# Optimization experiments

Measured on AMD Instinct MI355X. Metric: run time of the kernel, lower is better.

The kernel has to match this reference:

```python
import jax, jax.numpy as jnp
import numpy as np

LORA_SCALING = 16.0 / 8.0  # lora_alpha / lora_r


def setup_inputs() -> dict:
    key = jax.random.key(0)
    k_x, k_m, k_wm, k_bm, k_wa, k_wb = jax.random.split(key, 6)
    B, S, D_in, D_out, R = 4, 2048, 4096, 4096, 8
    x = jax.random.normal(k_x, (B, S, D_in), dtype=jnp.float32)
    im_mask = jax.random.randint(k_m, (B, S), 0, 2) > 0  # bool token mask
    # Linear weights stored torch-style: [out, in]
    W_main = jax.random.normal(k_wm, (D_out, D_in), dtype=jnp.float32) * (1.0 / np.sqrt(D_in))
    b_main = jax.random.normal(k_bm, (D_out,), dtype=jnp.float32) * 0.01
    W_A = jax.random.normal(k_wa, (R, D_in), dtype=jnp.float32) * (1.0 / np.sqrt(D_in))
    W_B = jax.random.normal(k_wb, (D_out, R), dtype=jnp.float32) * (1.0 / np.sqrt(R))
    return {"x": x, "im_mask": im_mask, "W_main": W_main, "b_main": b_main, "W_A": W_A, "W_B": W_B}


def reference(x, im_mask, W_main, b_main, W_A, W_B):
    # Main dense path: res = x @ W_main.T + b
    res = jnp.einsum('bsd,od->bso', x, W_main) + b_main
    # LoRA path applied only at masked tokens (dropout disabled / eval):
    # res[im_mask] += (x[im_mask] @ W_A.T) @ W_B.T * scaling
    # Static-shape equivalent: compute everywhere, mask the add.
    lora = jnp.einsum('bsr,or->bso', jnp.einsum('bsd,rd->bsr', x, W_A), W_B)
    return res + jnp.where(im_mask[..., None], lora * LORA_SCALING, jnp.zeros((), x.dtype))
```

## Files before the change

kernel.cpp:

```cpp
#include <hip/hip_runtime.h>

typedef unsigned short u16;
typedef unsigned int   u32;
typedef unsigned long long u64;
typedef __bf16 bf16x8 __attribute__((ext_vector_type(8)));
typedef float  f32x4  __attribute__((ext_vector_type(4)));

#define AS1 __attribute__((address_space(1)))
#define AS3 __attribute__((address_space(3)))

#define M_TOK 8192
#define K_DIM 4096
#define N_DIM 4096
#define BK    32
#define NKT   (K_DIM / BK)

static __device__ __forceinline__ u16 f2bf(float f) {
  u32 u = __builtin_bit_cast(u32, f);
  return (u16)((u + (0x7FFFu + ((u >> 16) & 1u))) >> 16);
}

static __device__ __forceinline__ void gld_lds16(const void* g, void* l) {
  __builtin_amdgcn_global_load_lds((AS1 u32*)(u64)g, (AS3 u32*)(u32)(u64)l, 16, 0, 0);
}

__global__ __launch_bounds__(256) void k_prep(const float* __restrict__ x,
                                              const float* __restrict__ WA,
                                              const float* __restrict__ W,
                                              u16* __restrict__ xb,
                                              float* __restrict__ mid,
                                              u16* __restrict__ Wb) {
  const int t = threadIdx.x;
  if (blockIdx.x >= M_TOK) {
    const int cb = blockIdx.x - M_TOK;
    const float4* W4 = (const float4*)W;
    ushort4* Wb4 = (ushort4*)Wb;
    const int n4 = (N_DIM * K_DIM) / 4;
    int i = cb * 256 + t;
    for (; i < n4; i += 2048 * 256) {
      float4 v = W4[i];
      ushort4 o;
      o.x = f2bf(v.x); o.y = f2bf(v.y); o.z = f2bf(v.z); o.w = f2bf(v.w);
      Wb4[i] = o;
    }
    return;
  }
  const int m = blockIdx.x;
  const float4* xr = (const float4*)(x + (size_t)m * K_DIM);
  ushort4* xbr = (ushort4*)(xb + (size_t)m * K_DIM);
  float a[8] = {0.f,0.f,0.f,0.f,0.f,0.f,0.f,0.f};
  #pragma unroll
  for (int i = 0; i < 4; ++i) {
    const int k4 = t + i * 256;
    float4 v = xr[k4];
    ushort4 o;
    o.x = f2bf(v.x); o.y = f2bf(v.y); o.z = f2bf(v.z); o.w = f2bf(v.w);
    xbr[k4] = o;
    #pragma unroll
    for (int r = 0; r < 8; ++r) {
      float4 wv = ((const float4*)(WA + (size_t)r * K_DIM))[k4];
      a[r] += v.x * wv.x + v.y * wv.y + v.z * wv.z + v.w * wv.w;
    }
  }
  #pragma unroll
  for (int r = 0; r < 8; ++r) {
    #pragma unroll
    for (int off = 32; off > 0; off >>= 1)
      a[r] += __shfl_down(a[r], off);
  }
  __shared__ float red[4][8];
  const int w = t >> 6, l = t & 63;
  if (l == 0) {
    #pragma unroll
    for (int r = 0; r < 8; ++r) red[w][r] = a[r];
  }
  __syncthreads();
  if (t < 8)
    mid[(size_t)m * 8 + t] = 2.0f * (red[0][t] + red[1][t] + red[2][t] + red[3][t]);
}

__global__ __launch_bounds__(512, 2) void k_gemm(
    const u16* __restrict__ A, const u16* __restrict__ B,
    const float* __restrict__ bias, const int* __restrict__ mask,
    const float* __restrict__ mid, const float* __restrict__ WBw,
    float* __restrict__ out) {
  __shared__ u16 smem[4][2][256][BK];

  const int t = threadIdx.x;
  const int wid = t >> 6, l = t & 63;
  const int wr = wid >> 2, wc = wid & 3;
  const int fr = l & 15, fq = l >> 4;

  const int bid = blockIdx.x;
  const int swz = (bid & 7) * 64 + (bid >> 3);
  const int bm = swz >> 4, bn = swz & 15;

  const char* Ag = (const char*)(A + (size_t)bm * 256 * K_DIM);
  const char* Bg = (const char*)(B + (size_t)bn * 256 * K_DIM);
  const size_t rowb = (size_t)K_DIM * 2;

  const int srow = t >> 2;
  const int schk = (((t & 3) ^ ((t >> 3) & 3)) * 16);
  const char* bA0 = Ag + (size_t)srow * rowb + schk;
  const char* bA1 = Ag + (size_t)(128 + srow) * rowb + schk;
  const char* bB0 = Bg + (size_t)srow * rowb + schk;
  const char* bB1 = Bg + (size_t)(128 + srow) * rowb + schk;
  char* lbase = (char*)&smem[0][0][0][0] + wid * 1024;

  f32x4 acc[8][4];
  #pragma unroll
  for (int m = 0; m < 8; ++m)
    #pragma unroll
    for (int n = 0; n < 4; ++n)
      acc[m][n] = (f32x4){0.f, 0.f, 0.f, 0.f};

  #pragma unroll
  for (int pk = 0; pk < 3; ++pk) {
    gld_lds16(bA0 + pk * 64, lbase + pk * 32768);
    gld_lds16(bA1 + pk * 64, lbase + pk * 32768 + 8192);
    gld_lds16(bB0 + pk * 64, lbase + pk * 32768 + 16384);
    gld_lds16(bB1 + pk * 64, lbase + pk * 32768 + 24576);
  }
  asm volatile("s_waitcnt vmcnt(4)" ::: "memory");
  __builtin_amdgcn_s_barrier();

  const int csw = (fq ^ ((fr >> 1) & 3)) * 8;

  const char* gA0 = bA0 + 192;
  const char* gA1 = bA1 + 192;
  const char* gB0 = bB0 + 192;
  const char* gB1 = bB1 + 192;

  bf16x8 af[8], bfP[4], bfQ[4];

  {
    const u16* Ap_ = &smem[0][0][wr * 128 + fr][csw];
    const u16* Bp_ = &smem[0][1][wc * 64 + fr][csw];
    #pragma unroll
    for (int m = 0; m < 8; ++m) af[m] = *(const bf16x8*)(Ap_ + m * 16 * BK);
    #pragma unroll
    for (int n = 0; n < 4; ++n) bfP[n] = *(const bf16x8*)(Bp_ + n * 16 * BK);
  }

  #define K_TILE(RBUF, SB, DOSTAGE, DOREAD, GOFF, WAIT, BFC, BFN) do {       \
    if (DOSTAGE) {                                                           \
      gld_lds16(gA0 + (GOFF), lbase + (SB) * 32768);                         \
      gld_lds16(gA1 + (GOFF), lbase + (SB) * 32768 + 8192);                  \
      gld_lds16(gB0 + (GOFF), lbase + (SB) * 32768 + 16384);                 \
      gld_lds16(gB1 + (GOFF), lbase + (SB) * 32768 + 24576);                 \
    }                                                                        \
    __builtin_amdgcn_s_setprio(1);                                           \
    _Pragma("unroll")                                                        \
    for (int m = 0; m < 4; ++m)                                              \
      _Pragma("unroll")                                                      \
      for (int n = 0; n < 4; ++n)                                            \
        acc[m][n] = __builtin_amdgcn_mfma_f32_16x16x32_bf16(                 \
            af[m], BFC[n], acc[m][n], 0, 0, 0);                              \
    __builtin_amdgcn_s_setprio(0);                                           \
    if (DOREAD) {                                                            \
      const u16* Ap_ = &smem[RBUF][0][wr * 128 + fr][csw];                   \
      const u16* Bp_ = &smem[RBUF][1][wc * 64 + fr][csw];                    \
      _Pragma("unroll")                                                      \
      for (int m = 0; m < 4; ++m)                                            \
        af[m] = *(const bf16x8*)(Ap_ + m * 16 * BK);                         \
      _Pragma("unroll")                                                      \
      for (int n = 0; n < 4; ++n)                                            \
        BFN[n] = *(const bf16x8*)(Bp_ + n * 16 * BK);                        \
    }                                                                        \
    __builtin_amdgcn_sched_barrier(0);                                       \
    __builtin_amdgcn_s_setprio(1);                                           \
    _Pragma("unroll")                                                        \
    for (int m = 4; m < 8; ++m)                                              \
      _Pragma("unroll")                                                      \
      for (int n = 0; n < 4; ++n)                                            \
        acc[m][n] = __builtin_amdgcn_mfma_f32_16x16x32_bf16(                 \
            af[m], BFC[n], acc[m][n], 0, 0, 0);                              \
    __builtin_amdgcn_s_setprio(0);                                           \
    if (DOREAD) {                                                            \
      const u16* Ap_ = &smem[RBUF][0][wr * 128 + fr][csw];                   \
      _Pragma("unroll")                                                      \
      for (int m = 4; m < 8; ++m)                                            \
        af[m] = *(const bf16x8*)(Ap_ + m * 16 * BK);                         \
    }                                                                        \
    __builtin_amdgcn_sched_barrier(0);                                       \
    WAIT;                                                                    \
    __builtin_amdgcn_s_barrier();                                            \
  } while (0)

  #define VM4 asm volatile("s_waitcnt vmcnt(4)" ::: "memory")
  #define VM0 asm volatile("s_waitcnt vmcnt(0)" ::: "memory")
  #define NOW ((void)0)

  for (int ktb = 0; ktb < NKT - 4; ktb += 4) {
    K_TILE(1, 3, true, true, 0,   VM4, bfP, bfQ);
    K_TILE(2, 0, true, true, 64,  VM4, bfQ, bfP);
    K_TILE(3, 1, true, true, 128, VM4, bfP, bfQ);
    K_TILE(0, 2, true, true, 192, VM4, bfQ, bfP);
    gA0 += 256; gA1 += 256; gB0 += 256; gB1 += 256;
  }
  K_TILE(1, 3, true,  true,  0, VM4, bfP, bfQ);
  K_TILE(2, 0, false, true,  0, VM0, bfQ, bfP);
  K_TILE(3, 0, false, true,  0, NOW, bfP, bfQ);
  K_TILE(0, 0, false, false, 0, NOW, bfQ, bfP);

  #undef K_TILE
  #undef VM4
  #undef VM0
  #undef NOW

  const int gn0 = bn * 256 + wc * 64;
  const size_t gm0 = (size_t)bm * 256 + wr * 128;
  float wbv[4][8]; float bv[4];
  #pragma unroll
  for (int n = 0; n < 4; ++n) {
    const int gn = gn0 + n * 16 + fr;
    bv[n] = bias[gn];
    const float4 w0 = ((const float4*)(WBw + (size_t)gn * 8))[0];
    const float4 w1 = ((const float4*)(WBw + (size_t)gn * 8))[1];
    wbv[n][0] = w0.x; wbv[n][1] = w0.y; wbv[n][2] = w0.z; wbv[n][3] = w0.w;
    wbv[n][4] = w1.x; wbv[n][5] = w1.y; wbv[n][6] = w1.z; wbv[n][7] = w1.w;
  }
  #pragma unroll
  for (int m = 0; m < 8; ++m) {
    #pragma unroll
    for (int j = 0; j < 4; ++j) {
      const size_t gm = gm0 + m * 16 + fq * 4 + j;
      const int msk = mask[gm];
      const float4 m0 = ((const float4*)(mid + gm * 8))[0];
      const float4 m1 = ((const float4*)(mid + gm * 8))[1];
      float* orow = out + gm * (size_t)N_DIM;
      #pragma unroll
      for (int n = 0; n < 4; ++n) {
        const float lora =
            m0.x * wbv[n][0] + m0.y * wbv[n][1] + m0.z * wbv[n][2] + m0.w * wbv[n][3] +
            m1.x * wbv[n][4] + m1.y * wbv[n][5] + m1.z * wbv[n][6] + m1.w * wbv[n][7];
        orow[gn0 + n * 16 + fr] = acc[m][n][j] + bv[n] + (msk ? lora : 0.0f);
      }
    }
  }
}

extern "C" void kernel_launch(void* const* d_in, const int* in_sizes, int n_in,
                              void* d_out, int out_size, void* d_ws, size_t ws_size,
                              hipStream_t stream) {
  (void)in_sizes; (void)n_in; (void)out_size; (void)ws_size;
  const float* x     = (const float*)d_in[0];
  const int*   mask  = (const int*)d_in[1];
  const float* Wm    = (const float*)d_in[2];
  const float* bmain = (const float*)d_in[3];
  const float* WA    = (const float*)d_in[4];
  const float* WB    = (const float*)d_in[5];
  float* out = (float*)d_out;

  u16* xb  = (u16*)d_ws;
  u16* wb  = xb + (size_t)M_TOK * K_DIM;
  float* mid = (float*)(wb + (size_t)N_DIM * K_DIM);

  k_prep<<<M_TOK + 2048, 256, 0, stream>>>(x, WA, Wm, xb, mid, wb);
  dim3 grid((M_TOK / 256) * (N_DIM / 256));
  k_gemm<<<grid, 512, 0, stream>>>(xb, wb, bmain, mask, mid, WB, out);
}
```

Baseline: 331.2 us.

## Load B fragments directly from global into registers, stage only A through LDS

Stops staging the B (weight) tile through shared memory. Each wave now loads its own B MFMA fragments straight from global memory into registers, two K-tiles ahead, while A keeps its 4-buffer LDS pipeline. This halves LDS footprint and LDS read traffic, which should ease LDS bandwidth pressure and the occupancy limit. In exchange B is no longer shared across the two wave rows, so global and L2 traffic for B doubles, and the vmcnt wait accounting changes, which risks stalls or ordering errors.

```diff
diff --git a/kernel.cpp b/kernel.cpp
--- a/kernel.cpp
+++ b/kernel.cpp
@@ -84,7 +84,7 @@
     const float* __restrict__ bias, const int* __restrict__ mask,
     const float* __restrict__ mid, const float* __restrict__ WBw,
     float* __restrict__ out) {
-  __shared__ u16 smem[4][2][256][BK];
+  __shared__ u16 smem[4][256][BK];
 
   const int t = threadIdx.x;
   const int wid = t >> 6, l = t & 63;
@@ -101,11 +101,11 @@
 
   const int srow = t >> 2;
   const int schk = (((t & 3) ^ ((t >> 3) & 3)) * 16);
-  const char* bA0 = Ag + (size_t)srow * rowb + schk;
-  const char* bA1 = Ag + (size_t)(128 + srow) * rowb + schk;
-  const char* bB0 = Bg + (size_t)srow * rowb + schk;
-  const char* bB1 = Bg + (size_t)(128 + srow) * rowb + schk;
-  char* lbase = (char*)&smem[0][0][0][0] + wid * 1024;
+  const char* gA0 = Ag + (size_t)srow * rowb + schk;
+  const char* gA1 = Ag + (size_t)(128 + srow) * rowb + schk;
+  char* lbase = (char*)&smem[0][0][0] + wid * 1024;
+
+  const char* qB = Bg + (size_t)(wc * 64 + fr) * rowb + fq * 16;
 
   f32x4 acc[8][4];
   #pragma unroll
@@ -114,41 +114,43 @@
     for (int n = 0; n < 4; ++n)
       acc[m][n] = (f32x4){0.f, 0.f, 0.f, 0.f};
 
+  bf16x8 af[8], bfA[4], bfB[4];
+
   #pragma unroll
   for (int pk = 0; pk < 3; ++pk) {
-    gld_lds16(bA0 + pk * 64, lbase + pk * 32768);
-    gld_lds16(bA1 + pk * 64, lbase + pk * 32768 + 8192);
-    gld_lds16(bB0 + pk * 64, lbase + pk * 32768 + 16384);
-    gld_lds16(bB1 + pk * 64, lbase + pk * 32768 + 24576);
-  }
+    gld_lds16(gA0 + pk * 64, lbase + pk * 16384);
+    gld_lds16(gA1 + pk * 64, lbase + pk * 16384 + 8192);
+  }
+  __builtin_amdgcn_sched_barrier(0);
+  #pragma unroll
+  for (int n = 0; n < 4; ++n)
+    bfA[n] = *(const bf16x8*)(qB + (size_t)n * 16 * rowb);
+  __builtin_amdgcn_sched_barrier(0);
+  #pragma unroll
+  for (int n = 0; n < 4; ++n)
+    bfB[n] = *(const bf16x8*)(qB + (size_t)n * 16 * rowb + 64);
+  __builtin_amdgcn_sched_barrier(0);
   asm volatile("s_waitcnt vmcnt(4)" ::: "memory");
   __builtin_amdgcn_s_barrier();
 
   const int csw = (fq ^ ((fr >> 1) & 3)) * 8;
 
-  const char* gA0 = bA0 + 192;
-  const char* gA1 = bA1 + 192;
-  const char* gB0 = bB0 + 192;
-  const char* gB1 = bB1 + 192;
-
-  bf16x8 af[8], bfP[4], bfQ[4];
-
   {
-    const u16* Ap_ = &smem[0][0][wr * 128 + fr][csw];
-    const u16* Bp_ = &smem[0][1][wc * 64 + fr][csw];
+    const u16* Ap_ = &smem[0][wr * 128 + fr][csw];
     #pragma unroll
     for (int m = 0; m < 8; ++m) af[m] = *(const bf16x8*)(Ap_ + m * 16 * BK);
-    #pragma unroll
-    for (int n = 0; n < 4; ++n) bfP[n] = *(const bf16x8*)(Bp_ + n * 16 * BK);
-  }
-
-  #define K_TILE(RBUF, SB, DOSTAGE, DOREAD, GOFF, WAIT, BFC, BFN) do {       \
+  }
+
+  const char* pA0 = gA0 + 192;
+  const char* pA1 = gA1 + 192;
+  const char* pB  = qB + 128;
+
+  #define K_TILE(RBUF, SB, DOSTAGE, DOREAD, DOB, GOFF, BOFF, WAIT, BFC) do { \
     if (DOSTAGE) {                                                           \
-      gld_lds16(gA0 + (GOFF), lbase + (SB) * 32768);                         \
-      gld_lds16(gA1 + (GOFF), lbase + (SB) * 32768 + 8192);                  \
-      gld_lds16(gB0 + (GOFF), lbase + (SB) * 32768 + 16384);                 \
-      gld_lds16(gB1 + (GOFF), lbase + (SB) * 32768 + 24576);                 \
-    }                                                                        \
+      gld_lds16(pA0 + (GOFF), lbase + (SB) * 16384);                         \
+      gld_lds16(pA1 + (GOFF), lbase + (SB) * 16384 + 8192);                  \
+    }                                                                        \
+    __builtin_amdgcn_sched_barrier(0);                                       \
     __builtin_amdgcn_s_setprio(1);                                           \
     _Pragma("unroll")                                                        \
     for (int m = 0; m < 4; ++m)                                              \
@@ -158,14 +160,10 @@
             af[m], BFC[n], acc[m][n], 0, 0, 0);                              \
     __builtin_amdgcn_s_setprio(0);                                           \
     if (DOREAD) {                                                            \
-      const u16* Ap_ = &smem[RBUF][0][wr * 128 + fr][csw];                   \
-      const u16* Bp_ = &smem[RBUF][1][wc * 64 + fr][csw];                    \
+      const u16* Ap_ = &smem[RBUF][wr * 128 + fr][csw];                      \
       _Pragma("unroll")                                                      \
       for (int m = 0; m < 4; ++m)                                            \
         af[m] = *(const bf16x8*)(Ap_ + m * 16 * BK);                         \
-      _Pragma("unroll")                                                      \
-      for (int n = 0; n < 4; ++n)                                            \
-        BFN[n] = *(const bf16x8*)(Bp_ + n * 16 * BK);                        \
     }                                                                        \
     __builtin_amdgcn_sched_barrier(0);                                       \
     __builtin_amdgcn_s_setprio(1);                                           \
@@ -177,33 +175,41 @@
             af[m], BFC[n], acc[m][n], 0, 0, 0);                              \
     __builtin_amdgcn_s_setprio(0);                                           \
     if (DOREAD) {                                                            \
-      const u16* Ap_ = &smem[RBUF][0][wr * 128 + fr][csw];                   \
+      const u16* Ap_ = &smem[RBUF][wr * 128 + fr][csw];                      \
       _Pragma("unroll")                                                      \
       for (int m = 4; m < 8; ++m)                                            \
         af[m] = *(const bf16x8*)(Ap_ + m * 16 * BK);                         \
+    }                                                                        \
+    __builtin_amdgcn_sched_barrier(0);                                       \
+    if (DOB) {                                                               \
+      _Pragma("unroll")                                                      \
+      for (int n = 0; n < 4; ++n)                                            \
+        BFC[n] = *(const bf16x8*)(pB + (size_t)n * 16 * rowb + (BOFF));      \
     }                                                                        \
     __builtin_amdgcn_sched_barrier(0);                                       \
     WAIT;                                                                    \
     __builtin_amdgcn_s_barrier();                                            \
   } while (0)
 
+  #define VM6 asm volatile("s_waitcnt vmcnt(6)" ::: "memory")
   #define VM4 asm volatile("s_waitcnt vmcnt(4)" ::: "memory")
   #define VM0 asm volatile("s_waitcnt vmcnt(0)" ::: "memory")
   #define NOW ((void)0)
 
   for (int ktb = 0; ktb < NKT - 4; ktb += 4) {
-    K_TILE(1, 3, true, true, 0,   VM4, bfP, bfQ);
-    K_TILE(2, 0, true, true, 64,  VM4, bfQ, bfP);
-    K_TILE(3, 1, true, true, 128, VM4, bfP, bfQ);
-    K_TILE(0, 2, true, true, 192, VM4, bfQ, bfP);
-    gA0 += 256; gA1 += 256; gB0 += 256; gB1 += 256;
-  }
-  K_TILE(1, 3, true,  true,  0, VM4, bfP, bfQ);
-  K_TILE(2, 0, false, true,  0, VM0, bfQ, bfP);
-  K_TILE(3, 0, false, true,  0, NOW, bfP, bfQ);
-  K_TILE(0, 0, false, false, 0, NOW, bfQ, bfP);
+    K_TILE(1, 3, true, true, true, 0,   0,   VM6, bfA);
+    K_TILE(2, 0, true, true, true, 64,  64,  VM6, bfB);
+    K_TILE(3, 1, true, true, true, 128, 128, VM6, bfA);
+    K_TILE(0, 2, true, true, true, 192, 192, VM6, bfB);
+    pA0 += 256; pA1 += 256; pB += 256;
+  }
+  K_TILE(1, 3, true,  true,  true,  0, 0,   VM6, bfA);
+  K_TILE(2, 0, false, true,  true,  0, 64,  VM4, bfB);
+  K_TILE(3, 1, false, true,  false, 0, 0,   VM0, bfA);
+  K_TILE(0, 2, false, false, false, 0, 0,   NOW, bfB);
 
   #undef K_TILE
+  #undef VM6
   #undef VM4
   #undef VM0
   #undef NOW
```

Result: slower. 458.1 us (+38.3%).
